# Optimization experiments

Hardware: AMD Instinct MI355X
Metric: run time of the kernel (lower is better)

## Reference

```python
import jax, jax.numpy as jnp
import numpy as np

WINDOW = (7, 7, 7)
DIM = 192
HEADS = 6
B_ = 256
NW = 32
N = int(np.prod(WINDOW))


def _relative_position_index(window_size):
    coords = np.stack(np.meshgrid(*[np.arange(w) for w in window_size], indexing='ij'))
    cf = coords.reshape(len(window_size), -1)  # (3, N)
    rel = cf[:, :, None] - cf[:, None, :]      # (3, N, N)
    rel = rel.transpose(1, 2, 0).copy()        # (N, N, 3)
    for i, w in enumerate(window_size):
        rel[:, :, i] += w - 1
    rel[:, :, 0] *= (2 * window_size[1] - 1) * (2 * window_size[2] - 1)
    rel[:, :, 1] *= 2 * window_size[2] - 1
    return rel.sum(-1).astype(np.int32)       # (N, N)


def setup_inputs() -> dict:
    key = jax.random.key(0)
    ks = jax.random.split(key, 8)
    table_rows = int(np.prod([2 * w - 1 for w in WINDOW]))  # 2197
    s = 0.02
    return {
        'skip': jax.random.normal(ks[0], (B_, N, DIM), jnp.float32),
        'x_up': jax.random.normal(ks[1], (B_, N, DIM), jnp.float32),
        'mask': jax.random.normal(ks[2], (NW, N, N), jnp.float32),
        'rel_index': jnp.asarray(_relative_position_index(WINDOW)),
        'table': s * jax.random.normal(ks[3], (table_rows, HEADS), jnp.float32),
        'kv_w': jax.random.normal(ks[4], (DIM, 2 * DIM), jnp.float32) / np.sqrt(DIM),
        'kv_b': jnp.zeros((2 * DIM,), jnp.float32),
        'proj_w': jax.random.normal(ks[5], (DIM, DIM), jnp.float32) / np.sqrt(DIM),
        'proj_b': jnp.zeros((DIM,), jnp.float32),
    }


def reference(skip, x_up, mask, rel_index, table, kv_w, kv_b, proj_w, proj_b):
    B, n, C = skip.shape
    H = HEADS
    D = C // H
    scale = D ** -0.5
    # kv projection: (B, N, 2C) -> k, v each (B, H, N, D)
    kv = skip @ kv_w + kv_b
    kv = kv.reshape(B, n, 2, H, D)
    k = kv[:, :, 0].transpose(0, 2, 1, 3)
    v = kv[:, :, 1].transpose(0, 2, 1, 3)
    q = (x_up.reshape(B, n, H, D).transpose(0, 2, 1, 3)) * scale
    attn = jnp.einsum('bhnd,bhmd->bhnm', q, k)  # (B, H, N, N)
    # gathered relative position bias: (N, N, H) -> (H, N, N)
    bias = table[rel_index].transpose(2, 0, 1)
    attn = attn + bias[None]
    nW = mask.shape[0]
    attn = attn.reshape(B // nW, nW, H, n, n) + mask[None, :, None]
    attn = jax.nn.softmax(attn.reshape(B, H, n, n), axis=-1)
    x = jnp.einsum('bhnm,bhmd->bhnd', attn, v)
    x = x.transpose(0, 2, 1, 3).reshape(B, n, C)
    return x @ proj_w + proj_b
```

## Files before the change

kernel.cpp:

```cpp
#include <hip/hip_runtime.h>
#include <hip/hip_bf16.h>

#define B_  256
#define N_  343
#define C_  192
#define H_  6
#define D_  32
#define NW_ 32
#define NN_ (N_*N_)
#define TROWS 2197
#define NP_ 352
#define PLANE (NP_*NP_)

typedef unsigned int  uint32;
typedef unsigned short u16;
typedef __attribute__((ext_vector_type(8))) short bf16x8;
typedef __attribute__((ext_vector_type(4))) float f32x4;

union frag8 { uint4 u4; bf16x8 h8; short s[8]; };

__device__ __forceinline__ float bf2f(u16 u){
  union { uint32 u; float f; } v; v.u = ((uint32)u) << 16; return v.f;
}
__device__ __forceinline__ u16 f2bf(float f){
  union { float f; uint32 u; } v; v.f = f;
  uint32 u = v.u;
  return (u16)((u + 0x7FFFu + ((u >> 16) & 1u)) >> 16);
}

__device__ __forceinline__ bool detect_f32(const uint32* w){
  int c = 0;
  #pragma unroll
  for (int u = 0; u < 32; u++){
    int e = (w[u*37] >> 7) & 0xFF;
    c += (e > 150);
  }
  return c >= 3;
}
__device__ __forceinline__ float ldf(const void* p, size_t i, bool f32){
  return f32 ? ((const float*)p)[i] : bf2f(((const u16*)p)[i]);
}
__device__ __forceinline__ void stf(void* p, size_t i, float v, bool f32){
  if (f32) ((float*)p)[i] = v;
  else     ((u16*)p)[i]   = f2bf(v);
}

__device__ __forceinline__ int klsidx(int j, int d){
  return j*32 + ((((d>>3) ^ ((j>>2)&3)))<<3) + (d&7);
}
__device__ __forceinline__ int vtidx(int d, int j){
  return d*352 + ((((j>>3) ^ ((d>>2)&3)))<<3) + (j&7);
}
__device__ __forceinline__ int plsidx(int row, int col){
  return row*32 + ((((col>>3) ^ ((row>>2)&3)))<<3) + (col&7);
}


__global__ void prep_bp(const void* __restrict__ skip, const int* __restrict__ rel,
                        const void* __restrict__ table, u16* __restrict__ bp){
  const bool F32 = detect_f32((const uint32*)skip);
  size_t gid = ((size_t)blockIdx.x*256 + threadIdx.x)*8;
  int p   = (int)(gid / PLANE);
  int rem = (int)(gid % PLANE);
  int i = rem / NP_, j0 = rem % NP_;
  frag8 o;
  #pragma unroll
  for (int m = 0; m < 8; m++){
    int j = j0 + m; float v = 0.f;
    if (i < N_ && j < N_){
      int r = rel[i*N_ + j];
      v = ldf(table, (size_t)r*H_ + p, F32);
    }
    o.s[m] = (short)f2bf(v);
  }
  *(uint4*)&bp[gid] = o.u4;
}

__global__ void prep_bm2(const void* __restrict__ skip, const void* __restrict__ mask,
                         const u16* __restrict__ bp, u16* __restrict__ bm){
  const bool F32 = detect_f32((const uint32*)skip);
  size_t gid = ((size_t)blockIdx.x*256 + threadIdx.x)*8;
  int pl  = (int)(gid / PLANE);
  int rem = (int)(gid % PLANE);
  int i = rem / NP_, j0 = rem % NP_;
  int w = pl / H_, h = pl % H_;
  frag8 bg; bg.u4 = *(const uint4*)&bp[(size_t)h*PLANE + rem];
  frag8 o;
  #pragma unroll
  for (int m = 0; m < 8; m++){
    int j = j0 + m;
    float v = bf2f((u16)bg.s[m]);
    if (i < N_ && j < N_) v += ldf(mask, (size_t)w*NN_ + (size_t)i*N_ + j, F32);
    o.s[m] = (short)f2bf(v);
  }
  *(uint4*)&bm[gid] = o.u4;
}

__global__ __launch_bounds__(512, 2) void kv_gemm2(
    const void* __restrict__ skip, const void* __restrict__ kv_w,
    const void* __restrict__ kv_b, u16* __restrict__ kvws){
  __shared__ __align__(16) u16 sk[32*200];
  const bool F32 = detect_f32((const uint32*)skip);
  const int b = blockIdx.x;
  const int t = threadIdx.x, lane = t & 63, wave = t >> 6;
  const int n16 = lane & 15, q = lane >> 4;

  float kvb[3];
  u16*  p3[3];
  int   d3[3], isK[3];
  frag8 bw[3][6];
  #pragma unroll
  for (int c3 = 0; c3 < 3; c3++){
    int col = (wave*3 + c3)*16 + n16;
    kvb[c3] = ldf(kv_b, col, F32);
    #pragma unroll
    for (int ks = 0; ks < 6; ks++)
      #pragma unroll
      for (int j = 0; j < 8; j++)
        bw[c3][ks].s[j] = (short)f2bf(ldf(kv_w, (size_t)(ks*32 + q*8 + j)*384 + col, F32));
    if (col < 192){
      int h = col >> 5; d3[c3] = col & 31; isK[c3] = 1;
      p3[c3] = kvws + (size_t)(b*H_ + h)*22528;
    } else {
      int cv = col - 192; int h = cv >> 5; d3[c3] = cv & 31; isK[c3] = 0;
      p3[c3] = kvws + (size_t)(b*H_ + h)*22528 + 11264;
    }
  }

  for (int rc = 0; rc < 11; rc++){
    __syncthreads();
    for (int u = t; u < 768; u += 512){
      int r = u / 24, cc = (u % 24)*8;
      int grow = rc*32 + r;
      uint4 vv;
      if (grow < N_){
        size_t g = ((size_t)b*N_ + grow)*C_ + cc;
        if (F32){
          const float* gp = (const float*)skip + g;
          float4 f0 = *(const float4*)gp, f1 = *(const float4*)(gp + 4);
          frag8 fv;
          fv.s[0]=(short)f2bf(f0.x); fv.s[1]=(short)f2bf(f0.y);
          fv.s[2]=(short)f2bf(f0.z); fv.s[3]=(short)f2bf(f0.w);
          fv.s[4]=(short)f2bf(f1.x); fv.s[5]=(short)f2bf(f1.y);
          fv.s[6]=(short)f2bf(f1.z); fv.s[7]=(short)f2bf(f1.w);
          vv = fv.u4;
        } else {
          vv = *(const uint4*)((const u16*)skip + g);
        }
      } else {
        vv = make_uint4(0,0,0,0);
      }
      *(uint4*)&sk[r*200 + cc] = vv;
    }
    __syncthreads();
    frag8 af[2][6];
    #pragma unroll
    for (int half = 0; half < 2; half++)
      #pragma unroll
      for (int ks = 0; ks < 6; ks++)
        af[half][ks].u4 = *(const uint4*)&sk[(half*16 + n16)*200 + ks*32 + q*8];
    #pragma unroll
    for (int c3 = 0; c3 < 3; c3++){
      #pragma unroll
      for (int half = 0; half < 2; half++){
        f32x4 acc = {0.f,0.f,0.f,0.f};
        #pragma unroll
        for (int ks = 0; ks < 6; ks++)
          acc = __builtin_amdgcn_mfma_f32_16x16x32_bf16(af[half][ks].h8, bw[c3][ks].h8, acc, 0,0,0);
        #pragma unroll
        for (int r = 0; r < 4; r++){
          int grow = rc*32 + half*16 + q*4 + r;
          u16 val = f2bf(acc[r] + kvb[c3]);
          if (isK[c3]) p3[c3][klsidx(grow, d3[c3])] = val;
          else         p3[c3][vtidx(d3[c3], grow)] = val;
        }
      }
    }
  }
}

#define A_KLS 4096
#define A_VT  15360
#define A_TOT 26624

__global__ __launch_bounds__(512, 6) void attn2(
    const void* __restrict__ skip, const void* __restrict__ x_up,
    const u16* __restrict__ bm, const u16* __restrict__ kvws,
    u16* __restrict__ xws, void* __restrict__ out){
  __shared__ __align__(16) u16 sm[A_TOT];
  const bool F32 = detect_f32((const uint32*)skip);
  const int bid = blockIdx.x;
  const int b = bid / H_, h = bid % H_;
  const int w = b & (NW_-1);
  const int t = threadIdx.x, lane = t & 63, wave = t >> 6;
  const int n16 = lane & 15, q = lane >> 4;

  {
    const uint4* src = (const uint4*)(kvws + (size_t)bid*22528);
    uint4* dst = (uint4*)&sm[A_KLS];
    for (int u = t; u < 2816; u += 512) dst[u] = src[u];
  }
  __syncthreads();

  const u16* bmp = bm + (size_t)(w*H_ + h)*PLANE;
  u16* pls = &sm[wave*512];
  const float SC = 0.17677669529663687f;

  for (int it = wave; it < 22; it += 8){
    int i0 = it*16;
    frag8 aq;
    {
      int qrow = min(i0 + n16, N_-1);
      size_t base = ((size_t)b*N_ + qrow)*C_ + h*D_ + q*8;
      if (F32){
        const float* xf = (const float*)x_up + base;
        float4 f0 = *(const float4*)xf, f1 = *(const float4*)(xf + 4);
        aq.s[0]=(short)f2bf(f0.x); aq.s[1]=(short)f2bf(f0.y);
        aq.s[2]=(short)f2bf(f0.z); aq.s[3]=(short)f2bf(f0.w);
        aq.s[4]=(short)f2bf(f1.x); aq.s[5]=(short)f2bf(f1.y);
        aq.s[6]=(short)f2bf(f1.z); aq.s[7]=(short)f2bf(f1.w);
      } else {
        aq.u4 = *(const uint4*)((const u16*)x_up + base);
      }
    }
    f32x4 O0 = {0.f,0.f,0.f,0.f}, O1 = {0.f,0.f,0.f,0.f};
    float lp[4] = {0.f,0.f,0.f,0.f};
    const int brow = lane >> 2, bc4 = lane & 3;
    const u16* bmrow = bmp + (size_t)(i0 + brow)*NP_ + bc4*8;
    const int pwr = brow*32 + ((bc4 ^ ((brow>>2)&3))<<3);
    uint4 nbm = *(const uint4*)bmrow;
    for (int jc = 0; jc < 11; jc++){
      int j0 = jc*32;
      uint4 bmv = nbm;
      if (jc < 10) nbm = *(const uint4*)(bmrow + j0 + 32);
      *(uint4*)&pls[pwr] = bmv;
      int ja = j0 + n16, jb = ja + 16;
      frag8 bk0, bk1;
      bk0.u4 = *(const uint4*)&sm[A_KLS + klsidx(ja, q*8)];
      bk1.u4 = *(const uint4*)&sm[A_KLS + klsidx(jb, q*8)];
      f32x4 z = {0.f,0.f,0.f,0.f};
      f32x4 s0 = __builtin_amdgcn_mfma_f32_16x16x32_bf16(aq.h8, bk0.h8, z, 0,0,0);
      f32x4 s1 = __builtin_amdgcn_mfma_f32_16x16x32_bf16(aq.h8, bk1.h8, z, 0,0,0);
      #pragma unroll
      for (int r = 0; r < 4; r++){
        int row_ = q*4 + r;
        float bma = bf2f(pls[plsidx(row_, n16)]);
        float bmb = bf2f(pls[plsidx(row_, 16 + n16)]);
        float pa = (ja < N_) ? __expf(fmaf(s0[r], SC, bma)) : 0.f;
        float pb = (jb < N_) ? __expf(fmaf(s1[r], SC, bmb)) : 0.f;
        lp[r] += pa + pb;
        pls[plsidx(row_, n16)]      = f2bf(pa);
        pls[plsidx(row_, 16 + n16)] = f2bf(pb);
      }
      frag8 ap; ap.u4 = *(const uint4*)&pls[plsidx(n16, q*8)];
      frag8 bv0, bv1;
      bv0.u4 = *(const uint4*)&sm[A_VT + vtidx(n16,      j0 + q*8)];
      bv1.u4 = *(const uint4*)&sm[A_VT + vtidx(16 + n16, j0 + q*8)];
      O0 = __builtin_amdgcn_mfma_f32_16x16x32_bf16(ap.h8, bv0.h8, O0, 0,0,0);
      O1 = __builtin_amdgcn_mfma_f32_16x16x32_bf16(ap.h8, bv1.h8, O1, 0,0,0);
    }
    #pragma unroll
    for (int msk = 1; msk < 16; msk <<= 1){
      #pragma unroll
      for (int r = 0; r < 4; r++) lp[r] += __shfl_xor(lp[r], msk, 64);
    }
    #pragma unroll
    for (int r = 0; r < 4; r++){
      int i = i0 + q*4 + r;
      if (i < N_){
        float rl = 1.f / lp[r];
        if (xws){
          u16* xp = xws + ((size_t)(b*H_ + h)*N_ + i)*D_;
          xp[n16]      = f2bf(O0[r]*rl);
          xp[16 + n16] = f2bf(O1[r]*rl);
        } else {
          size_t ob = ((size_t)b*N_ + i)*C_ + h*D_;
          stf(out, ob + n16,      O0[r]*rl, F32);
          stf(out, ob + 16 + n16, O1[r]*rl, F32);
        }
      }
    }
  }
}

__global__ __launch_bounds__(256, 4) void proj3(const u16* __restrict__ xws,
                                                void* __restrict__ outp,
                                                const void* __restrict__ pw,
                                                const void* __restrict__ pb,
                                                const void* __restrict__ skip){
  __shared__ __align__(16) u16 xs[64*200];
  const bool F32 = detect_f32((const uint32*)skip);
  const int t = threadIdx.x, lane = t & 63, wave = t >> 6;
  const int n16 = lane & 15, q = lane >> 4;
  const size_t row0 = (size_t)blockIdx.x * 64;

  for (int u = t; u < 1536; u += 256){
    int r = u / 24, c8 = u % 24;
    int g = (int)row0 + r;
    int b = g / N_, i = g - b*N_;
    int h = c8 >> 2, d0 = (c8 & 3)*8;
    uint4 vv = *(const uint4*)&xws[((size_t)(b*H_ + h)*N_ + i)*D_ + d0];
    *(uint4*)&xs[r*200 + h*32 + d0] = vv;
  }
  frag8 bwf[3][6];
  float pbv[3];
  #pragma unroll
  for (int c3 = 0; c3 < 3; c3++){
    int col = (wave*3 + c3)*16 + n16;
    pbv[c3] = ldf(pb, col, F32);
    #pragma unroll
    for (int ks = 0; ks < 6; ks++)
      #pragma unroll
      for (int j = 0; j < 8; j++)
        bwf[c3][ks].s[j] = (short)f2bf(ldf(pw, (size_t)(ks*32 + q*8 + j)*C_ + col, F32));
  }
  __syncthreads();
  for (int rt = 0; rt < 4; rt++){
    frag8 af[6];
    #pragma unroll
    for (int ks = 0; ks < 6; ks++)
      af[ks].u4 = *(const uint4*)&xs[(rt*16 + n16)*200 + ks*32 + q*8];
    #pragma unroll
    for (int c3 = 0; c3 < 3; c3++){
      f32x4 acc = {0.f,0.f,0.f,0.f};
      #pragma unroll
      for (int ks = 0; ks < 6; ks++)
        acc = __builtin_amdgcn_mfma_f32_16x16x32_bf16(af[ks].h8, bwf[c3][ks].h8, acc, 0,0,0);
      int col = (wave*3 + c3)*16 + n16;
      #pragma unroll
      for (int r = 0; r < 4; r++)
        stf(outp, (row0 + rt*16 + q*4 + r)*C_ + col, acc[r] + pbv[c3], F32);
    }
  }
}


__global__ void prep_biasg(const void* __restrict__ skip, const int* __restrict__ rel,
                           const void* __restrict__ table, u16* __restrict__ biasg){
  const bool F32 = detect_f32((const uint32*)skip);
  int idx = blockIdx.x*256 + threadIdx.x;
  if (idx >= NN_) return;
  int r = rel[idx];
  #pragma unroll
  for (int h = 0; h < H_; h++)
    biasg[(size_t)h*NN_ + idx] = f2bf(ldf(table, (size_t)r*H_ + h, F32));
}

#define KLS_OFF 6400
#define VT_OFF  (KLS_OFF + 352*40)
#define SMEM_U16 (VT_OFF + 32*360)

__global__ __launch_bounds__(512, 4) void attn_fused(
    const void* __restrict__ skip, const void* __restrict__ x_up,
    const void* __restrict__ mask, const u16* __restrict__ biasg,
    const void* __restrict__ kv_w, const void* __restrict__ kv_b,
    void* __restrict__ out){
  __shared__ __align__(16) u16 sm[SMEM_U16];
  const bool F32 = detect_f32((const uint32*)skip);
  const int bid = blockIdx.x;
  const int b = bid / H_, h = bid % H_;
  const int w = b & (NW_-1);
  const int t = threadIdx.x;
  const int lane = t & 63, wave = t >> 6;
  const int n16 = lane & 15, q = lane >> 4;
  const int colt = wave & 3;
  const int half = wave >> 2;
  const int gcol = (colt < 2) ? (h*D_ + colt*16 + n16)
                              : (C_ + h*D_ + (colt-2)*16 + n16);
  const float kvb = ldf(kv_b, gcol, F32);
  frag8 bw[6];
  #pragma unroll
  for (int ks = 0; ks < 6; ks++)
    #pragma unroll
    for (int j = 0; j < 8; j++)
      bw[ks].s[j] = (short)f2bf(ldf(kv_w, (size_t)(ks*32 + q*8 + j)*384 + gcol, F32));

  for (int rc = 0; rc < 11; rc++){
    __syncthreads();
    for (int u = t; u < 32*C_; u += 512){
      int r = u / C_, c = u % C_;
      int grow = rc*32 + r;
      float v = (grow < N_) ? ldf(skip, ((size_t)b*N_ + grow)*C_ + c, F32) : 0.f;
      sm[r*200 + c] = f2bf(v);
    }
    __syncthreads();
    f32x4 acc = {0.f, 0.f, 0.f, 0.f};
    #pragma unroll
    for (int ks = 0; ks < 6; ks++){
      frag8 a;  a.u4 = *(const uint4*)&sm[(half*16 + n16)*200 + ks*32 + q*8];
      acc = __builtin_amdgcn_mfma_f32_16x16x32_bf16(a.h8, bw[ks].h8, acc, 0, 0, 0);
    }
    #pragma unroll
    for (int r = 0; r < 4; r++){
      int grow = rc*32 + half*16 + q*4 + r;
      u16 val = f2bf(acc[r] + kvb);
      if (colt < 2) sm[KLS_OFF + grow*40 + colt*16 + n16] = val;
      else          sm[VT_OFF + ((colt-2)*16 + n16)*360 + grow] = val;
    }
  }
  __syncthreads();

  const float scale = 0.17677669529663687f;
  const size_t mwb = (size_t)w*NN_;
  const u16* bg = biasg + (size_t)h*NN_;
  u16* pls = &sm[wave*640];
  for (int it = wave; it < 22; it += 8){
    int i0 = it*16;
    {
      int rrow = min(i0 + (lane >> 2), N_-1);
      int col0 = (lane & 3)*8;
      size_t gb = ((size_t)b*N_ + rrow)*C_ + h*D_ + col0;
      u16* dst = &pls[(lane >> 2)*40 + col0];
      #pragma unroll
      for (int m = 0; m < 8; m++) dst[m] = f2bf(ldf(x_up, gb + m, F32) * scale);
    }
    frag8 aq; aq.u4 = *(const uint4*)&pls[n16*40 + q*8];
    f32x4 O0 = {0.f,0.f,0.f,0.f}, O1 = {0.f,0.f,0.f,0.f};
    float lp[4] = {0.f, 0.f, 0.f, 0.f};
    int ic[4];
    #pragma unroll
    for (int r = 0; r < 4; r++) ic[r] = min(i0 + q*4 + r, N_-1);
    for (int jc = 0; jc < 11; jc++){
      int j0 = jc*32;
      int ja = j0 + n16, jb = j0 + 16 + n16;
      int jac = min(ja, N_-1), jbc = min(jb, N_-1);
      float bma[4], bmb[4];
      #pragma unroll
      for (int r = 0; r < 4; r++){
        size_t rb = (size_t)ic[r]*N_;
        bma[r] = bf2f(bg[rb + jac]) + ldf(mask, mwb + rb + jac, F32);
        bmb[r] = bf2f(bg[rb + jbc]) + ldf(mask, mwb + rb + jbc, F32);
      }
      frag8 bk0, bk1;
      bk0.u4 = *(const uint4*)&sm[KLS_OFF + (j0 + n16)*40 + q*8];
      bk1.u4 = *(const uint4*)&sm[KLS_OFF + (j0 + 16 + n16)*40 + q*8];
      f32x4 z = {0.f,0.f,0.f,0.f};
      f32x4 s0 = __builtin_amdgcn_mfma_f32_16x16x32_bf16(aq.h8, bk0.h8, z, 0,0,0);
      f32x4 s1 = __builtin_amdgcn_mfma_f32_16x16x32_bf16(aq.h8, bk1.h8, z, 0,0,0);
      #pragma unroll
      for (int r = 0; r < 4; r++){
        float pa = (ja < N_) ? __expf(s0[r] + bma[r] - 12.f) : 0.f;
        float pb = (jb < N_) ? __expf(s1[r] + bmb[r] - 12.f) : 0.f;
        lp[r] += pa + pb;
        pls[(q*4 + r)*40 + n16]      = f2bf(pa);
        pls[(q*4 + r)*40 + 16 + n16] = f2bf(pb);
      }
      frag8 ap; ap.u4 = *(const uint4*)&pls[n16*40 + q*8];
      frag8 bv0, bv1;
      bv0.u4 = *(const uint4*)&sm[VT_OFF + n16*360 + j0 + q*8];
      bv1.u4 = *(const uint4*)&sm[VT_OFF + (16 + n16)*360 + j0 + q*8];
      O0 = __builtin_amdgcn_mfma_f32_16x16x32_bf16(ap.h8, bv0.h8, O0, 0,0,0);
      O1 = __builtin_amdgcn_mfma_f32_16x16x32_bf16(ap.h8, bv1.h8, O1, 0,0,0);
    }
    #pragma unroll
    for (int msk = 1; msk < 16; msk <<= 1){
      #pragma unroll
      for (int r = 0; r < 4; r++) lp[r] += __shfl_xor(lp[r], msk, 64);
    }
    #pragma unroll
    for (int r = 0; r < 4; r++){
      int i = i0 + q*4 + r;
      if (i < N_){
        float rl = 1.f / lp[r];
        size_t ob = ((size_t)b*N_ + i)*C_ + h*D_;
        stf(out, ob + n16,      O0[r]*rl, F32);
        stf(out, ob + 16 + n16, O1[r]*rl, F32);
      }
    }
  }
}

__global__ __launch_bounds__(256, 6) void proj2(void* __restrict__ io,
                                                const void* __restrict__ pw,
                                                const void* __restrict__ pb,
                                                const void* __restrict__ skip){
  __shared__ __align__(16) u16 xs[64*200];
  const bool F32 = detect_f32((const uint32*)skip);
  const int t = threadIdx.x;
  const int lane = t & 63, wave = t >> 6;
  const int n16 = lane & 15, q = lane >> 4;
  const size_t row0 = (size_t)blockIdx.x * 64;

  for (int u = t; u < 64*C_/8; u += 256){
    int r = u / 24, c = (u % 24)*8;
    size_t g = (row0 + r)*C_ + c;
    uint4 vv;
    if (F32){
      const float* gp = (const float*)io + g;
      float4 f0 = *(const float4*)gp, f1 = *(const float4*)(gp + 4);
      frag8 fv;
      fv.s[0]=(short)f2bf(f0.x); fv.s[1]=(short)f2bf(f0.y);
      fv.s[2]=(short)f2bf(f0.z); fv.s[3]=(short)f2bf(f0.w);
      fv.s[4]=(short)f2bf(f1.x); fv.s[5]=(short)f2bf(f1.y);
      fv.s[6]=(short)f2bf(f1.z); fv.s[7]=(short)f2bf(f1.w);
      vv = fv.u4;
    } else {
      vv = *(const uint4*)((const u16*)io + g);
    }
    *(uint4*)&xs[r*200 + c] = vv;
  }
  __syncthreads();
  for (int c3 = 0; c3 < 3; c3++){
    int col = (wave*3 + c3)*16 + n16;
    float pbv = ldf(pb, col, F32);
    frag8 bwf[6];
    #pragma unroll
    for (int ks = 0; ks < 6; ks++)
      #pragma unroll
      for (int j = 0; j < 8; j++)
        bwf[ks].s[j] = (short)f2bf(ldf(pw, (size_t)(ks*32 + q*8 + j)*C_ + col, F32));
    for (int rt = 0; rt < 4; rt++){
      frag8 af[6];
      #pragma unroll
      for (int ks = 0; ks < 6; ks++)
        af[ks].u4 = *(const uint4*)&xs[(rt*16 + n16)*200 + ks*32 + q*8];
      f32x4 acc = {0.f,0.f,0.f,0.f};
      #pragma unroll
      for (int ks = 0; ks < 6; ks++)
        acc = __builtin_amdgcn_mfma_f32_16x16x32_bf16(af[ks].h8, bwf[ks].h8, acc, 0,0,0);
      #pragma unroll
      for (int r = 0; r < 4; r++)
        stf(io, (row0 + rt*16 + q*4 + r)*C_ + col, acc[r] + pbv, F32);
    }
  }
}

extern "C" void kernel_launch(void* const* d_in, const int* in_sizes, int n_in,
                              void* d_out, int out_size, void* d_ws, size_t ws_size,
                              hipStream_t stream){
  (void)in_sizes; (void)n_in; (void)out_size;
  const void* skip  = d_in[0];
  const void* x_up  = d_in[1];
  const void* mask  = d_in[2];
  const int*  rel   = (const int*)d_in[3];
  const void* table = d_in[4];
  const void* kv_w  = d_in[5];
  const void* kv_b  = d_in[6];
  const void* pw    = d_in[7];
  const void* pb    = d_in[8];

  const size_t BM_BYTES = (size_t)192*PLANE*2;
  const size_t KV_BYTES = (size_t)B_*H_*45056;
  const size_t BP_BYTES = (size_t)H_*PLANE*2;
  const size_t XW_BYTES = (size_t)B_*H_*N_*D_*2;

  if (ws_size >= BM_BYTES + KV_BYTES + XW_BYTES){
    u16* bm   = (u16*)d_ws;
    u16* kvws = (u16*)((char*)d_ws + BM_BYTES);
    u16* xws  = (u16*)((char*)d_ws + BM_BYTES + KV_BYTES);
    u16* bp   = xws;
    prep_bp <<<(H_*PLANE/8)/256, 256, 0, stream>>>(skip, rel, table, bp);
    prep_bm2<<<(192*PLANE/8)/256, 256, 0, stream>>>(skip, mask, bp, bm);
    kv_gemm2<<<B_, 512, 0, stream>>>(skip, kv_w, kv_b, kvws);
    attn2   <<<B_*H_, 512, 0, stream>>>(skip, x_up, bm, kvws, xws, d_out);
    proj3   <<<87808/64, 256, 0, stream>>>(xws, d_out, pw, pb, skip);
  } else if (ws_size >= BM_BYTES + KV_BYTES + BP_BYTES){
    u16* bm   = (u16*)d_ws;
    u16* kvws = (u16*)((char*)d_ws + BM_BYTES);
    u16* bp   = (u16*)((char*)d_ws + BM_BYTES + KV_BYTES);
    prep_bp <<<(H_*PLANE/8)/256, 256, 0, stream>>>(skip, rel, table, bp);
    prep_bm2<<<(192*PLANE/8)/256, 256, 0, stream>>>(skip, mask, bp, bm);
    kv_gemm2<<<B_, 512, 0, stream>>>(skip, kv_w, kv_b, kvws);
    attn2   <<<B_*H_, 512, 0, stream>>>(skip, x_up, bm, kvws, nullptr, d_out);
    proj2   <<<87808/64, 256, 0, stream>>>(d_out, pw, pb, skip);
  } else {
    u16* biasg = (u16*)d_ws;
    prep_biasg<<<(NN_+255)/256, 256, 0, stream>>>(skip, rel, table, biasg);
    attn_fused<<<B_*H_, 512, 0, stream>>>(skip, x_up, mask, biasg, kv_w, kv_b, d_out);
    proj2     <<<87808/64, 256, 0, stream>>>(d_out, pw, pb, skip);
  }
}
```

Before: 462.4 us.

## Compute transposed scores in attention to drop LDS round-trip; split kv GEMM blocks

The attention loop now computes S^T (K as the A operand) so each lane holds a column of probabilities. The P fragment for the PV MFMA is rebuilt with packed bf16 conversion and lane shuffles, which removes the per-wave LDS staging of the bias/mask tile and probabilities. The bias/mask is prescaled by log2e so the loop can use exp2f with a folded scale. The kv GEMM is split into two blocks per batch with 16-row chunks and register prefetch of the next chunk, which raises occupancy and overlaps loads with MFMA work. The cost is more shuffles, bias loads straight from global memory in the inner loop, and redundant recomputation of the kv weight fragments across twice as many blocks.

```diff
diff --git a/kernel.cpp b/kernel.cpp
--- a/kernel.cpp
+++ b/kernel.cpp
@@ -51,8 +51,22 @@
 __device__ __forceinline__ int vtidx(int d, int j){
   return d*352 + ((((j>>3) ^ ((d>>2)&3)))<<3) + (j&7);
 }
-__device__ __forceinline__ int plsidx(int row, int col){
-  return row*32 + ((((col>>3) ^ ((row>>2)&3)))<<3) + (col&7);
+
+__device__ __forceinline__ uint4 ld_row8(const void* __restrict__ src, bool F32,
+                                         int b, int grow, int col){
+  if (grow >= N_) return make_uint4(0,0,0,0);
+  size_t g = ((size_t)b*N_ + grow)*C_ + col;
+  if (F32){
+    const float* gp = (const float*)src + g;
+    float4 f0 = *(const float4*)gp, f1 = *(const float4*)(gp + 4);
+    frag8 fv;
+    fv.s[0]=(short)f2bf(f0.x); fv.s[1]=(short)f2bf(f0.y);
+    fv.s[2]=(short)f2bf(f0.z); fv.s[3]=(short)f2bf(f0.w);
+    fv.s[4]=(short)f2bf(f1.x); fv.s[5]=(short)f2bf(f1.y);
+    fv.s[6]=(short)f2bf(f1.z); fv.s[7]=(short)f2bf(f1.w);
+    return fv.u4;
+  }
+  return *(const uint4*)((const u16*)src + g);
 }
 
 
@@ -79,6 +93,7 @@
 __global__ void prep_bm2(const void* __restrict__ skip, const void* __restrict__ mask,
                          const u16* __restrict__ bp, u16* __restrict__ bm){
   const bool F32 = detect_f32((const uint32*)skip);
+  const float LOG2E = 1.4426950408889634f;
   size_t gid = ((size_t)blockIdx.x*256 + threadIdx.x)*8;
   int pl  = (int)(gid / PLANE);
   int rem = (int)(gid % PLANE);
@@ -91,17 +106,19 @@
     int j = j0 + m;
     float v = bf2f((u16)bg.s[m]);
     if (i < N_ && j < N_) v += ldf(mask, (size_t)w*NN_ + (size_t)i*N_ + j, F32);
-    o.s[m] = (short)f2bf(v);
+    o.s[m] = (short)f2bf(v * LOG2E);
   }
   *(uint4*)&bm[gid] = o.u4;
 }
 
-__global__ __launch_bounds__(512, 2) void kv_gemm2(
+__global__ __launch_bounds__(512, 4) void kv_gemm3(
     const void* __restrict__ skip, const void* __restrict__ kv_w,
     const void* __restrict__ kv_b, u16* __restrict__ kvws){
-  __shared__ __align__(16) u16 sk[32*200];
-  const bool F32 = detect_f32((const uint32*)skip);
-  const int b = blockIdx.x;
+  __shared__ __align__(16) u16 sk[16*200];
+  const bool F32 = detect_f32((const uint32*)skip);
+  const int bx = blockIdx.x;
+  const int b = bx >> 1, half_ = bx & 1;
+  const int rb0 = half_ * 176;
   const int t = threadIdx.x, lane = t & 63, wave = t >> 6;
   const int n16 = lane & 15, q = lane >> 4;
 
@@ -127,67 +144,45 @@
     }
   }
 
+  const bool stg = (t < 384);
+  const int sr = t / 24, sc8 = (t % 24) * 8;
+  uint4 pre = make_uint4(0,0,0,0);
+  if (stg) pre = ld_row8(skip, F32, b, rb0 + sr, sc8);
+
   for (int rc = 0; rc < 11; rc++){
     __syncthreads();
-    for (int u = t; u < 768; u += 512){
-      int r = u / 24, cc = (u % 24)*8;
-      int grow = rc*32 + r;
-      uint4 vv;
-      if (grow < N_){
-        size_t g = ((size_t)b*N_ + grow)*C_ + cc;
-        if (F32){
-          const float* gp = (const float*)skip + g;
-          float4 f0 = *(const float4*)gp, f1 = *(const float4*)(gp + 4);
-          frag8 fv;
-          fv.s[0]=(short)f2bf(f0.x); fv.s[1]=(short)f2bf(f0.y);
-          fv.s[2]=(short)f2bf(f0.z); fv.s[3]=(short)f2bf(f0.w);
-          fv.s[4]=(short)f2bf(f1.x); fv.s[5]=(short)f2bf(f1.y);
-          fv.s[6]=(short)f2bf(f1.z); fv.s[7]=(short)f2bf(f1.w);
-          vv = fv.u4;
-        } else {
-          vv = *(const uint4*)((const u16*)skip + g);
-        }
-      } else {
-        vv = make_uint4(0,0,0,0);
-      }
-      *(uint4*)&sk[r*200 + cc] = vv;
-    }
+    if (stg) *(uint4*)&sk[sr*200 + sc8] = pre;
     __syncthreads();
-    frag8 af[2][6];
-    #pragma unroll
-    for (int half = 0; half < 2; half++)
+    if (rc < 10 && stg) pre = ld_row8(skip, F32, b, rb0 + (rc+1)*16 + sr, sc8);
+    frag8 af[6];
+    #pragma unroll
+    for (int ks = 0; ks < 6; ks++)
+      af[ks].u4 = *(const uint4*)&sk[n16*200 + ks*32 + q*8];
+    #pragma unroll
+    for (int c3 = 0; c3 < 3; c3++){
+      f32x4 acc = {0.f,0.f,0.f,0.f};
       #pragma unroll
       for (int ks = 0; ks < 6; ks++)
-        af[half][ks].u4 = *(const uint4*)&sk[(half*16 + n16)*200 + ks*32 + q*8];
-    #pragma unroll
-    for (int c3 = 0; c3 < 3; c3++){
-      #pragma unroll
-      for (int half = 0; half < 2; half++){
-        f32x4 acc = {0.f,0.f,0.f,0.f};
-        #pragma unroll
-        for (int ks = 0; ks < 6; ks++)
-          acc = __builtin_amdgcn_mfma_f32_16x16x32_bf16(af[half][ks].h8, bw[c3][ks].h8, acc, 0,0,0);
-        #pragma unroll
-        for (int r = 0; r < 4; r++){
-          int grow = rc*32 + half*16 + q*4 + r;
-          u16 val = f2bf(acc[r] + kvb[c3]);
-          if (isK[c3]) p3[c3][klsidx(grow, d3[c3])] = val;
-          else         p3[c3][vtidx(d3[c3], grow)] = val;
-        }
-      }
-    }
-  }
-}
-
-#define A_KLS 4096
-#define A_VT  15360
-#define A_TOT 26624
+        acc = __builtin_amdgcn_mfma_f32_16x16x32_bf16(af[ks].h8, bw[c3][ks].h8, acc, 0,0,0);
+      #pragma unroll
+      for (int r = 0; r < 4; r++){
+        int grow = rb0 + rc*16 + q*4 + r;
+        u16 val = f2bf(acc[r] + kvb[c3]);
+        if (isK[c3]) p3[c3][klsidx(grow, d3[c3])] = val;
+        else         p3[c3][vtidx(d3[c3], grow)] = val;
+      }
+    }
+  }
+}
+
+#define A2_VT  11264
+#define A2_TOT 22528
 
 __global__ __launch_bounds__(512, 6) void attn2(
     const void* __restrict__ skip, const void* __restrict__ x_up,
     const u16* __restrict__ bm, const u16* __restrict__ kvws,
     u16* __restrict__ xws, void* __restrict__ out){
-  __shared__ __align__(16) u16 sm[A_TOT];
+  __shared__ __align__(16) u16 sm[A2_TOT];
   const bool F32 = detect_f32((const uint32*)skip);
   const int bid = blockIdx.x;
   const int b = bid / H_, h = bid % H_;
@@ -197,17 +192,17 @@
 
   {
     const uint4* src = (const uint4*)(kvws + (size_t)bid*22528);
-    uint4* dst = (uint4*)&sm[A_KLS];
+    uint4* dst = (uint4*)sm;
     for (int u = t; u < 2816; u += 512) dst[u] = src[u];
   }
   __syncthreads();
 
   const u16* bmp = bm + (size_t)(w*H_ + h)*PLANE;
-  u16* pls = &sm[wave*512];
-  const float SC = 0.17677669529663687f;
+  const float SC2 = 0.17677669529663687f * 1.4426950408889634f;
 
   for (int it = wave; it < 22; it += 8){
     int i0 = it*16;
+    const u16* bmr = bmp + (size_t)(i0 + n16)*NP_;
     frag8 aq;
     {
       int qrow = min(i0 + n16, N_-1);
@@ -224,51 +219,58 @@
       }
     }
     f32x4 O0 = {0.f,0.f,0.f,0.f}, O1 = {0.f,0.f,0.f,0.f};
-    float lp[4] = {0.f,0.f,0.f,0.f};
-    const int brow = lane >> 2, bc4 = lane & 3;
-    const u16* bmrow = bmp + (size_t)(i0 + brow)*NP_ + bc4*8;
-    const int pwr = brow*32 + ((bc4 ^ ((brow>>2)&3))<<3);
-    uint4 nbm = *(const uint4*)bmrow;
+    float lp = 0.f;
     for (int jc = 0; jc < 11; jc++){
       int j0 = jc*32;
-      uint4 bmv = nbm;
-      if (jc < 10) nbm = *(const uint4*)(bmrow + j0 + 32);
-      *(uint4*)&pls[pwr] = bmv;
-      int ja = j0 + n16, jb = ja + 16;
+      uint2 mba = *(const uint2*)&bmr[j0 + q*4];
+      uint2 mbb = *(const uint2*)&bmr[j0 + 16 + q*4];
       frag8 bk0, bk1;
-      bk0.u4 = *(const uint4*)&sm[A_KLS + klsidx(ja, q*8)];
-      bk1.u4 = *(const uint4*)&sm[A_KLS + klsidx(jb, q*8)];
+      bk0.u4 = *(const uint4*)&sm[klsidx(j0 + n16, q*8)];
+      bk1.u4 = *(const uint4*)&sm[klsidx(j0 + 16 + n16, q*8)];
       f32x4 z = {0.f,0.f,0.f,0.f};
-      f32x4 s0 = __builtin_amdgcn_mfma_f32_16x16x32_bf16(aq.h8, bk0.h8, z, 0,0,0);
-      f32x4 s1 = __builtin_amdgcn_mfma_f32_16x16x32_bf16(aq.h8, bk1.h8, z, 0,0,0);
+      f32x4 s0 = __builtin_amdgcn_mfma_f32_16x16x32_bf16(bk0.h8, aq.h8, z, 0,0,0);
+      f32x4 s1 = __builtin_amdgcn_mfma_f32_16x16x32_bf16(bk1.h8, aq.h8, z, 0,0,0);
+      union { uint2 v; u16 e[4]; } Ua, Ub;
+      Ua.v = mba; Ub.v = mbb;
+      float pa[4], pb[4];
       #pragma unroll
       for (int r = 0; r < 4; r++){
-        int row_ = q*4 + r;
-        float bma = bf2f(pls[plsidx(row_, n16)]);
-        float bmb = bf2f(pls[plsidx(row_, 16 + n16)]);
-        float pa = (ja < N_) ? __expf(fmaf(s0[r], SC, bma)) : 0.f;
-        float pb = (jb < N_) ? __expf(fmaf(s1[r], SC, bmb)) : 0.f;
-        lp[r] += pa + pb;
-        pls[plsidx(row_, n16)]      = f2bf(pa);
-        pls[plsidx(row_, 16 + n16)] = f2bf(pb);
-      }
-      frag8 ap; ap.u4 = *(const uint4*)&pls[plsidx(n16, q*8)];
+        pa[r] = exp2f(fmaf(s0[r], SC2, bf2f(Ua.e[r])));
+        float eb = exp2f(fmaf(s1[r], SC2, bf2f(Ub.e[r])));
+        pb[r] = (j0 + 16 + q*4 + r < N_) ? eb : 0.f;
+        lp += pa[r] + pb[r];
+      }
+      uint32 A0, A1, B0, B1;
+      asm("v_cvt_pk_bf16_f32 %0, %1, %2" : "=v"(A0) : "v"(pa[0]), "v"(pa[1]));
+      asm("v_cvt_pk_bf16_f32 %0, %1, %2" : "=v"(A1) : "v"(pa[2]), "v"(pa[3]));
+      asm("v_cvt_pk_bf16_f32 %0, %1, %2" : "=v"(B0) : "v"(pb[0]), "v"(pb[1]));
+      asm("v_cvt_pk_bf16_f32 %0, %1, %2" : "=v"(B1) : "v"(pb[2]), "v"(pb[3]));
+      int src0 = ((q & 1) << 5) + n16;
+      int src1 = src0 + 16;
+      uint32 a0s = (uint32)__shfl((int)A0, src0), a1s = (uint32)__shfl((int)A1, src0);
+      uint32 a2s = (uint32)__shfl((int)A0, src1), a3s = (uint32)__shfl((int)A1, src1);
+      uint32 b0s = (uint32)__shfl((int)B0, src0), b1s = (uint32)__shfl((int)B1, src0);
+      uint32 b2s = (uint32)__shfl((int)B0, src1), b3s = (uint32)__shfl((int)B1, src1);
+      bool lo = (q < 2);
+      frag8 ap;
+      ap.u4.x = lo ? a0s : b0s;
+      ap.u4.y = lo ? a1s : b1s;
+      ap.u4.z = lo ? a2s : b2s;
+      ap.u4.w = lo ? a3s : b3s;
       frag8 bv0, bv1;
-      bv0.u4 = *(const uint4*)&sm[A_VT + vtidx(n16,      j0 + q*8)];
-      bv1.u4 = *(const uint4*)&sm[A_VT + vtidx(16 + n16, j0 + q*8)];
+      bv0.u4 = *(const uint4*)&sm[A2_VT + vtidx(n16,      j0 + q*8)];
+      bv1.u4 = *(const uint4*)&sm[A2_VT + vtidx(16 + n16, j0 + q*8)];
       O0 = __builtin_amdgcn_mfma_f32_16x16x32_bf16(ap.h8, bv0.h8, O0, 0,0,0);
       O1 = __builtin_amdgcn_mfma_f32_16x16x32_bf16(ap.h8, bv1.h8, O1, 0,0,0);
     }
-    #pragma unroll
-    for (int msk = 1; msk < 16; msk <<= 1){
-      #pragma unroll
-      for (int r = 0; r < 4; r++) lp[r] += __shfl_xor(lp[r], msk, 64);
-    }
+    lp += __shfl_xor(lp, 16);
+    lp += __shfl_xor(lp, 32);
     #pragma unroll
     for (int r = 0; r < 4; r++){
-      int i = i0 + q*4 + r;
+      int il = q*4 + r;
+      float rl = 1.f / __shfl(lp, (lane & 48) | il);
+      int i = i0 + il;
       if (i < N_){
-        float rl = 1.f / lp[r];
         if (xws){
           u16* xp = xws + ((size_t)(b*H_ + h)*N_ + i)*D_;
           xp[n16]      = f2bf(O0[r]*rl);
@@ -551,7 +553,7 @@
     u16* bp   = xws;
     prep_bp <<<(H_*PLANE/8)/256, 256, 0, stream>>>(skip, rel, table, bp);
     prep_bm2<<<(192*PLANE/8)/256, 256, 0, stream>>>(skip, mask, bp, bm);
-    kv_gemm2<<<B_, 512, 0, stream>>>(skip, kv_w, kv_b, kvws);
+    kv_gemm3<<<B_*2, 512, 0, stream>>>(skip, kv_w, kv_b, kvws);
     attn2   <<<B_*H_, 512, 0, stream>>>(skip, x_up, bm, kvws, xws, d_out);
     proj3   <<<87808/64, 256, 0, stream>>>(xws, d_out, pw, pb, skip);
   } else if (ws_size >= BM_BYTES + KV_BYTES + BP_BYTES){
@@ -560,7 +562,7 @@
     u16* bp   = (u16*)((char*)d_ws + BM_BYTES + KV_BYTES);
     prep_bp <<<(H_*PLANE/8)/256, 256, 0, stream>>>(skip, rel, table, bp);
     prep_bm2<<<(192*PLANE/8)/256, 256, 0, stream>>>(skip, mask, bp, bm);
-    kv_gemm2<<<B_, 512, 0, stream>>>(skip, kv_w, kv_b, kvws);
+    kv_gemm3<<<B_*2, 512, 0, stream>>>(skip, kv_w, kv_b, kvws);
     attn2   <<<B_*H_, 512, 0, stream>>>(skip, x_up, bm, kvws, nullptr, d_out);
     proj2   <<<87808/64, 256, 0, stream>>>(d_out, pw, pb, skip);
   } else {
```

Measured after the change: 509.7 us. 10.2% more time.
